# Optimization experiments

Measured on AMD Instinct MI355X. Metric: run time of the kernel, lower is better.

The kernel has to match this reference:

```python
import jax, jax.numpy as jnp
import numpy as np

# Static module configuration (RT-DETR defaults, 640x640 input pyramid)
SPATIAL_SHAPES = ((80, 80), (40, 40), (20, 20))
N_HEADS = 8
N_LEVELS = 3
N_POINTS = 4
D_MODEL = 256
HEAD_DIM = D_MODEL // N_HEADS
OFFSET_SCALE = 0.5
LP = N_LEVELS * N_POINTS


def setup_inputs() -> dict:
    key = jax.random.key(0)
    ks = jax.random.split(key, 10)
    B, Q = 16, 300
    S = sum(h * w for h, w in SPATIAL_SHAPES)  # 8400

    def w(k, shape, scale=0.02):
        return jax.random.normal(k, shape, jnp.float32) * scale

    return {
        "hidden_states": jax.random.normal(ks[0], (B, Q, D_MODEL), jnp.float32),
        "encoder_hidden_states": jax.random.normal(ks[1], (B, S, D_MODEL), jnp.float32),
        # (cx, cy, w, h) boxes in (0,1); 4-coordinate RTDETRv2 path
        "reference_points": jax.random.uniform(ks[2], (B, Q, 1, 4), jnp.float32, 0.1, 0.9),
        "w_value": w(ks[3], (D_MODEL, D_MODEL)),
        "b_value": jnp.zeros((D_MODEL,), jnp.float32),
        "w_offsets": w(ks[4], (N_HEADS * LP * 2, D_MODEL)),
        "b_offsets": w(ks[5], (N_HEADS * LP * 2,), 0.5),
        "w_attn": w(ks[6], (N_HEADS * LP, D_MODEL)),
        "b_attn": jnp.zeros((N_HEADS * LP,), jnp.float32),
        "w_out": w(ks[7], (D_MODEL, D_MODEL)),
        "b_out": jnp.zeros((D_MODEL,), jnp.float32),
    }


def _bilinear_sample(img, gx, gy):
    """grid_sample(mode=bilinear, padding_mode=zeros, align_corners=False).
    img: [N, C, H, W]; gx, gy: [N, Q, P] absolute pixel coords (already W*loc-0.5).
    Returns [N, Q, P, C]."""
    N, C, H, W = img.shape
    x0 = jnp.floor(gx)
    y0 = jnp.floor(gy)
    x1 = x0 + 1.0
    y1 = y0 + 1.0
    wx1 = gx - x0
    wx0 = 1.0 - wx1
    wy1 = gy - y0
    wy0 = 1.0 - wy1
    b = jnp.arange(N)[:, None, None]

    def gather(ix, iy):
        valid = (ix >= 0) & (ix < W) & (iy >= 0) & (iy < H)
        ixc = jnp.clip(ix, 0, W - 1).astype(jnp.int32)
        iyc = jnp.clip(iy, 0, H - 1).astype(jnp.int32)
        v = img[b, :, iyc, ixc]  # [N,Q,P,C]
        return v * valid[..., None].astype(img.dtype)

    return (gather(x0, y0) * (wx0 * wy0)[..., None]
            + gather(x1, y0) * (wx1 * wy0)[..., None]
            + gather(x0, y1) * (wx0 * wy1)[..., None]
            + gather(x1, y1) * (wx1 * wy1)[..., None])


def _msda_v2(hidden_states, encoder_hidden_states, reference_points,
             w_value, b_value, w_offsets, b_offsets, w_attn, b_attn, w_out, b_out):
    B, Q, _ = hidden_states.shape
    S = encoder_hidden_states.shape[1]

    value = (encoder_hidden_states @ w_value.T + b_value).reshape(B, S, N_HEADS, HEAD_DIM)
    offsets = (hidden_states @ w_offsets.T + b_offsets).reshape(B, Q, N_HEADS, LP, 2)
    attn = jax.nn.softmax(
        (hidden_states @ w_attn.T + b_attn).reshape(B, Q, N_HEADS, LP), axis=-1)

    # n_points_scale = [1/P]*L*P; 4-coordinate reference points (cx,cy,w,h)
    n_points_scale = jnp.float32(1.0 / N_POINTS)
    offset = offsets * n_points_scale * reference_points[:, :, None, :, 2:] * OFFSET_SCALE
    loc = reference_points[:, :, None, :, :2] + offset  # [B,Q,H,LP,2] in (0,1)

    # head-major value: [B*H, hd, S]
    v = value.transpose(0, 2, 3, 1).reshape(B * N_HEADS, HEAD_DIM, S)
    grids = loc.transpose(0, 2, 1, 3, 4).reshape(B * N_HEADS, Q, LP, 2)

    sampled = []
    start = 0
    for lvl, (H, W) in enumerate(SPATIAL_SHAPES):
        vl = v[:, :, start:start + H * W].reshape(B * N_HEADS, HEAD_DIM, H, W)
        g = grids[:, :, lvl * N_POINTS:(lvl + 1) * N_POINTS, :]
        # torch: grid = 2*loc-1 with align_corners=False -> pixel = loc*W - 0.5
        gx = g[..., 0] * W - 0.5
        gy = g[..., 1] * H - 0.5
        sampled.append(_bilinear_sample(vl, gx, gy))  # [B*H, Q, P, hd]
        start += H * W

    sv = jnp.concatenate(sampled, axis=2)  # [B*H, Q, LP, hd]
    aw = attn.transpose(0, 2, 1, 3).reshape(B * N_HEADS, Q, LP, 1)
    out = (sv * aw).sum(axis=2)  # [B*H, Q, hd]
    out = out.reshape(B, N_HEADS, Q, HEAD_DIM).transpose(0, 2, 1, 3).reshape(B, Q, D_MODEL)
    return out @ w_out.T + b_out


def reference(hidden_states, encoder_hidden_states, reference_points,
              w_value, b_value, w_offsets, b_offsets, w_attn, b_attn, w_out, b_out):
    return _msda_v2(hidden_states, encoder_hidden_states, reference_points,
                    w_value, b_value, w_offsets, b_offsets, w_attn, b_attn, w_out, b_out)
```

## Files before the change

### kernel.cpp

```cpp
#include <hip/hip_runtime.h>


typedef __attribute__((ext_vector_type(8))) short short8;
typedef __attribute__((ext_vector_type(4))) float f32x4;

__device__ __forceinline__ unsigned short f2bf(float f) {
    union { float f; unsigned int i; } v; v.f = f;
    unsigned int r = v.i + 0x7FFFu + ((v.i >> 16) & 1u);
    return (unsigned short)(r >> 16);
}
__device__ __forceinline__ float bf2f(unsigned short u) {
    union { unsigned int i; float f; } v;
    v.i = ((unsigned int)u) << 16;
    return v.f;
}
__device__ __forceinline__ short8 cvt8(const float* p) {
    f32x4 x = *(const f32x4*)p;
    f32x4 y = *(const f32x4*)(p + 4);
    short8 r;
#pragma unroll
    for (int q = 0; q < 4; ++q) {
        r[q]     = (short)f2bf(x[q]);
        r[q + 4] = (short)f2bf(y[q]);
    }
    return r;
}
__device__ __forceinline__ void barrier_lgkm() {
    asm volatile("s_waitcnt lgkmcnt(0)\n\ts_barrier" ::: "memory");
}

__global__ __launch_bounds__(256) void prep_kernel(
    const float* __restrict__ wv, const float* __restrict__ wo,
    const float* __restrict__ w_off, const float* __restrict__ w_attn,
    short8* __restrict__ wv_s, short8* __restrict__ wo_s, short8* __restrict__ wp_s)
{
    const int blk = blockIdx.x, tid = threadIdx.x;
    if (blk < 64) {
        const float* W = (blk < 32) ? wv : wo;
        short8* out    = (blk < 32) ? wv_s : wo_s;
        int s   = ((blk & 31) << 8) + tid;
        int kcb = s >> 10, sl = s & 1023;
        int n = ((sl >> 6) << 4) + (sl & 15);
        int k = (kcb << 5) + (((sl >> 4) & 3) << 3);
        out[s] = cvt8(W + n * 256 + k);
    } else {
        int s   = ((blk - 64) << 8) + tid;
        int kcb = s / 1152, sl = s - kcb * 1152;
        int n = ((sl >> 6) << 4) + (sl & 15);
        int k = (kcb << 5) + (((sl >> 4) & 3) << 3);
        const float* p = (n < 192) ? (w_off + (size_t)n * 256 + k)
                                   : (w_attn + (size_t)(n - 192) * 256 + k);
        wp_s[s] = cvt8(p);
    }
}

__global__ __launch_bounds__(256) void gemm128(
    const float* __restrict__ A,
    const short8* __restrict__ Wswz,
    const float* __restrict__ bias,
    unsigned short* __restrict__ C)
{
    __shared__ short8 lb[1024];
    const int tid  = threadIdx.x;
    const int wave = tid >> 6;
    const int lane = tid & 63;
    const int row0 = (blockIdx.x >> 1) * 128;
    const int colt = blockIdx.x & 1;
    const int mq   = wave >> 1;
    const int nq   = wave & 1;

    f32x4 acc[4][4];
#pragma unroll
    for (int i = 0; i < 4; ++i)
#pragma unroll
        for (int j = 0; j < 4; ++j) acc[i][j] = (f32x4){0.f, 0.f, 0.f, 0.f};

    const int sa0 = tid, sa1 = tid + 256;
    const int am0 = row0 + ((sa0 >> 6) << 4) + (sa0 & 15);
    const int ak0 = ((sa0 >> 4) & 3) << 3;
    const int am1 = row0 + ((sa1 >> 6) << 4) + (sa1 & 15);
    const int ak1 = ((sa1 >> 4) & 3) << 3;

    for (int kcb = 0; kcb < 8; ++kcb) {
        const int kc = kcb << 5;
        barrier_lgkm();
        lb[sa0] = cvt8(A + (size_t)am0 * 256 + kc + ak0);
        lb[sa1] = cvt8(A + (size_t)am1 * 256 + kc + ak1);
        const short8* wsrc = Wswz + (kcb << 10) + (colt << 9);
        lb[512 + tid]       = wsrc[tid];
        lb[768 + tid]       = wsrc[tid + 256];
        barrier_lgkm();

        short8 af[4], bf[4];
#pragma unroll
        for (int i = 0; i < 4; ++i) af[i] = lb[((mq << 2) + i) * 64 + lane];
#pragma unroll
        for (int j = 0; j < 4; ++j) bf[j] = lb[512 + ((nq << 2) + j) * 64 + lane];
#pragma unroll
        for (int i = 0; i < 4; ++i)
#pragma unroll
            for (int j = 0; j < 4; ++j)
                acc[i][j] = __builtin_amdgcn_mfma_f32_16x16x32_bf16(af[i], bf[j], acc[i][j], 0, 0, 0);
    }

    const int ncol = lane & 15;
    const int rsub = (lane >> 4) << 2;
#pragma unroll
    for (int i = 0; i < 4; ++i) {
        const int rb = row0 + ((mq << 2) + i) * 16 + rsub;
#pragma unroll
        for (int j = 0; j < 4; ++j) {
            const int n = (colt << 7) + ((nq << 2) + j) * 16 + ncol;
            const float bv = bias[n];
#pragma unroll
            for (int r = 0; r < 4; ++r)
                C[(size_t)(rb + r) * 256 + n] = f2bf(acc[i][j][r] + bv);
        }
    }
}

template <bool A_BF16, bool OUT_BF16>
__global__ __launch_bounds__(256) void gemm_nt(
    const void* __restrict__ Av,
    const short8* __restrict__ Wswz,
    const float* __restrict__ bias,
    void* __restrict__ Cv)
{
    __shared__ short8 lb[2048];
    const int tid  = threadIdx.x;
    const int wave = tid >> 6;
    const int lane = tid & 63;
    const int row0 = blockIdx.x * 64 + wave * 16;

    f32x4 acc[16];
#pragma unroll
    for (int t = 0; t < 16; ++t) acc[t] = (f32x4){0.f, 0.f, 0.f, 0.f};

    const int am = row0 + (lane & 15);
    const int kq = (lane >> 4) << 3;

    const unsigned short* Ab = (const unsigned short*)Av;
    const float*          Af = (const float*)Av;

    short8 acur[2], anext[2];
#pragma unroll
    for (int kk = 0; kk < 2; ++kk) {
        if (A_BF16) acur[kk] = *(const short8*)(Ab + (size_t)am * 256 + (kk << 5) + kq);
        else        acur[kk] = cvt8(Af + (size_t)am * 256 + (kk << 5) + kq);
    }

    for (int st = 0; st < 4; ++st) {
        barrier_lgkm();
#pragma unroll
        for (int i = 0; i < 8; ++i) {
            int s = tid + (i << 8);
            lb[s] = Wswz[(st << 11) + s];
        }
        barrier_lgkm();

        if (st < 3) {
            int kc = (st + 1) << 6;
#pragma unroll
            for (int kk = 0; kk < 2; ++kk) {
                if (A_BF16) anext[kk] = *(const short8*)(Ab + (size_t)am * 256 + kc + (kk << 5) + kq);
                else        anext[kk] = cvt8(Af + (size_t)am * 256 + kc + (kk << 5) + kq);
            }
        }

#pragma unroll
        for (int t = 0; t < 16; ++t) {
            short8 b0 = lb[t * 64 + lane];
            acc[t] = __builtin_amdgcn_mfma_f32_16x16x32_bf16(acur[0], b0, acc[t], 0, 0, 0);
            short8 b1 = lb[1024 + t * 64 + lane];
            acc[t] = __builtin_amdgcn_mfma_f32_16x16x32_bf16(acur[1], b1, acc[t], 0, 0, 0);
        }
        acur[0] = anext[0];
        acur[1] = anext[1];
    }

    const int ncol = lane & 15;
    const int rb   = row0 + ((lane >> 4) << 2);
#pragma unroll
    for (int t = 0; t < 16; ++t) {
        int n = (t << 4) + ncol;
        float bv = bias[n];
#pragma unroll
        for (int r = 0; r < 4; ++r) {
            float v = acc[t][r] + bv;
            if (OUT_BF16)
                ((unsigned short*)Cv)[(size_t)(rb + r) * 256 + n] = f2bf(v);
            else
                ((float*)Cv)[(size_t)(rb + r) * 256 + n] = v;
        }
    }
}

#define LGS 296
__global__ __launch_bounds__(256) void proj_gemm(
    const float* __restrict__ hidden,
    const short8* __restrict__ Wswz,
    const float* __restrict__ b_off, const float* __restrict__ b_attn,
    const float* __restrict__ refp,
    float* __restrict__ attnw, float* __restrict__ locw)
{
    __shared__ char smem[32 * LGS * 4];
    short8* lb = (short8*)smem;
    float*  lg = (float*)smem;

    const int tid  = threadIdx.x;
    const int wave = tid >> 6;
    const int lane = tid & 63;
    const int rq0  = blockIdx.x * 32;
    const int rg   = wave >> 1;
    const int ts   = (wave & 1) * 9;
    const int row0 = rq0 + rg * 16;

    f32x4 acc[9];
#pragma unroll
    for (int t = 0; t < 9; ++t) acc[t] = (f32x4){0.f, 0.f, 0.f, 0.f};

    const int am = row0 + (lane & 15);
    const int kq = (lane >> 4) << 3;

    for (int kcb = 0; kcb < 8; ++kcb) {
        __syncthreads();
#pragma unroll
        for (int i = 0; i < 5; ++i) {
            int s = tid + (i << 8);
            if (s < 1152) lb[s] = Wswz[kcb * 1152 + s];
        }
        __syncthreads();

        short8 a = cvt8(hidden + (size_t)am * 256 + (kcb << 5) + kq);
#pragma unroll
        for (int t = 0; t < 9; ++t)
            acc[t] = __builtin_amdgcn_mfma_f32_16x16x32_bf16(a, lb[(ts + t) * 64 + lane], acc[t], 0, 0, 0);
    }

    __syncthreads();
    const int ncol = lane & 15;
    const int rb   = rg * 16 + ((lane >> 4) << 2);
#pragma unroll
    for (int t = 0; t < 9; ++t) {
        int n = (ts + t) * 16 + ncol;
        float bv = (n < 192) ? b_off[n] : b_attn[n - 192];
#pragma unroll
        for (int r = 0; r < 4; ++r)
            lg[(rb + r) * LGS + n] = acc[t][r] + bv;
    }
    __syncthreads();

    {
        int r = tid >> 3, h = tid & 7;
        const float* lrow = lg + r * LGS + 192 + h * 12;
        float m = -1e30f;
#pragma unroll
        for (int p = 0; p < 12; ++p) m = fmaxf(m, lrow[p]);
        float e[12], sum = 0.f;
#pragma unroll
        for (int p = 0; p < 12; ++p) { e[p] = __expf(lrow[p] - m); sum += e[p]; }
        float inv = 1.f / sum;
        float* ao = attnw + (size_t)(rq0 + r) * 96 + h * 12;
#pragma unroll
        for (int p = 0; p < 12; ++p) ao[p] = e[p] * inv;
    }
    if (tid < 192) {
        int xy = tid & 1;
        for (int r = 0; r < 32; ++r) {
            int rq = rq0 + r;
            float rc  = refp[(size_t)rq * 4 + xy];
            float rwh = refp[(size_t)rq * 4 + 2 + xy];
            locw[(size_t)rq * 192 + tid] = rc + lg[r * LGS + tid] * 0.125f * rwh;
        }
    }
}

__global__ __launch_bounds__(256) void sample_kernel(
    const unsigned short* __restrict__ value,
    const float* __restrict__ attnw, const float* __restrict__ locw,
    unsigned short* __restrict__ sampled)
{
    const int rq  = blockIdx.x;
    const int b   = rq / 300;
    const int tid = threadIdx.x;

    __shared__ int4   soff[96];
    __shared__ float4 swt[96];

    if (tid < 96) {
        int h = tid / 12, lp = tid - h * 12;
        int l = lp >> 2;
        int Wl = (l == 0) ? 80 : (l == 1) ? 40 : 20;
        int s0 = (l == 0) ? 0  : (l == 1) ? 6400 : 8000;
        float lx = locw[(size_t)rq * 192 + h * 24 + lp * 2];
        float ly = locw[(size_t)rq * 192 + h * 24 + lp * 2 + 1];
        float aw = attnw[(size_t)rq * 96 + h * 12 + lp];
        float gx = lx * (float)Wl - 0.5f;
        float gy = ly * (float)Wl - 0.5f;
        float x0f = floorf(gx), y0f = floorf(gy);
        int   x0 = (int)x0f,   y0 = (int)y0f;
        float wx1 = gx - x0f, wx0 = 1.f - wx1;
        float wy1 = gy - y0f, wy0 = 1.f - wy1;
        int4 of; float4 wt;
#pragma unroll
        for (int j = 0; j < 4; ++j) {
            int x = x0 + (j & 1), y = y0 + (j >> 1);
            bool ok = (x >= 0) & (x < Wl) & (y >= 0) & (y < Wl);
            int idx = ok ? (((b * 8400 + s0 + y * Wl + x) * 8 + h) * 32) : 0;
            float w = ok ? aw * ((j & 1) ? wx1 : wx0) * ((j >> 1) ? wy1 : wy0) : 0.f;
            ((int*)&of)[j] = idx;
            ((float*)&wt)[j] = w;
        }
        soff[tid] = of;
        swt[tid]  = wt;
    }
    __syncthreads();

    const int h = tid >> 5, c = tid & 31;
    float acc = 0.f;
#pragma unroll
    for (int lp = 0; lp < 12; ++lp) {
        int idx = h * 12 + lp;
        int4   of = soff[idx];
        float4 wt = swt[idx];
        acc += wt.x * bf2f(value[of.x + c]);
        acc += wt.y * bf2f(value[of.y + c]);
        acc += wt.z * bf2f(value[of.z + c]);
        acc += wt.w * bf2f(value[of.w + c]);
    }
    sampled[(size_t)rq * 256 + tid] = f2bf(acc);
}

extern "C" void kernel_launch(void* const* d_in, const int* in_sizes, int n_in,
                              void* d_out, int out_size, void* d_ws, size_t ws_size,
                              hipStream_t stream)
{
    const float* hidden  = (const float*)d_in[0];
    const float* enc     = (const float*)d_in[1];
    const float* refp    = (const float*)d_in[2];
    const float* w_value = (const float*)d_in[3];
    const float* b_value = (const float*)d_in[4];
    const float* w_off   = (const float*)d_in[5];
    const float* b_off   = (const float*)d_in[6];
    const float* w_attn  = (const float*)d_in[7];
    const float* b_attn  = (const float*)d_in[8];
    const float* w_out   = (const float*)d_in[9];
    const float* b_out   = (const float*)d_in[10];

    char* ws = (char*)d_ws;
    unsigned short* value   = (unsigned short*)ws;
    unsigned short* sampled = (unsigned short*)(ws + 68812800);
    float*          attnw   = (float*)(ws + 71270400);
    float*          locw    = (float*)(ws + 73113600);
    short8*         wv_swz  = (short8*)(ws + 76800000);
    short8*         wo_swz  = (short8*)(ws + 76931072);
    short8*         wp_swz  = (short8*)(ws + 77062144);

    prep_kernel<<<100, 256, 0, stream>>>(w_value, w_out, w_off, w_attn,
                                         wv_swz, wo_swz, wp_swz);
    gemm128<<<2100, 256, 0, stream>>>(enc, wv_swz, b_value, value);
    proj_gemm<<<150, 256, 0, stream>>>(hidden, wp_swz, b_off, b_attn,
                                       refp, attnw, locw);
    sample_kernel<<<4800, 256, 0, stream>>>(value, attnw, locw, sampled);
    gemm_nt<true, false><<<75, 256, 0, stream>>>(sampled, wo_swz, b_out,
                                                 d_out);
}
```

Measured before the change: 298.6 us.

## Prefetch next A tile into registers and load weights directly into LDS

In the bf16 MFMA projection GEMM, the fp32 A-tile loads for the next k-block are issued into registers before the current block's MFMAs. The pre-swizzled weight tile is moved with global_load_lds DMA instead of going through registers. Hand-written s_waitcnt vmcnt counts let the prefetch stay in flight across the barrier. This is meant to hide global load latency in the K loop, at the cost of fragile manual waitcnt accounting and more registers in use.

```diff
diff --git a/kernel.cpp b/kernel.cpp
--- a/kernel.cpp
+++ b/kernel.cpp
@@ -25,8 +25,22 @@
     }
     return r;
 }
+__device__ __forceinline__ short8 pack8(f32x4 x, f32x4 y) {
+    short8 r;
+#pragma unroll
+    for (int q = 0; q < 4; ++q) {
+        r[q]     = (short)f2bf(x[q]);
+        r[q + 4] = (short)f2bf(y[q]);
+    }
+    return r;
+}
 __device__ __forceinline__ void barrier_lgkm() {
     asm volatile("s_waitcnt lgkmcnt(0)\n\ts_barrier" ::: "memory");
+}
+__device__ __forceinline__ void gload_lds16(const void* g, void* l) {
+    __builtin_amdgcn_global_load_lds(
+        (const __attribute__((address_space(1))) void*)g,
+        (__attribute__((address_space(3))) void*)l, 16, 0, 0);
 }
 
 __global__ __launch_bounds__(256) void prep_kernel(
@@ -81,15 +95,41 @@
     const int am1 = row0 + ((sa1 >> 6) << 4) + (sa1 & 15);
     const int ak1 = ((sa1 >> 4) & 3) << 3;
 
+    const float* pa0 = A + (size_t)am0 * 256 + ak0;
+    const float* pa1 = A + (size_t)am1 * 256 + ak1;
+
+    f32x4 a00 = *(const f32x4*)(pa0);
+    f32x4 a01 = *(const f32x4*)(pa0 + 4);
+    f32x4 a10 = *(const f32x4*)(pa1);
+    f32x4 a11 = *(const f32x4*)(pa1 + 4);
+
+    const int wv64 = wave << 6;
+    const short8* wcol = Wswz + (colt << 9);
+    short8* ldsB0 = &lb[512 + wv64];
+    short8* ldsB1 = &lb[768 + wv64];
+
     for (int kcb = 0; kcb < 8; ++kcb) {
-        const int kc = kcb << 5;
-        barrier_lgkm();
-        lb[sa0] = cvt8(A + (size_t)am0 * 256 + kc + ak0);
-        lb[sa1] = cvt8(A + (size_t)am1 * 256 + kc + ak1);
-        const short8* wsrc = Wswz + (kcb << 10) + (colt << 9);
-        lb[512 + tid]       = wsrc[tid];
-        lb[768 + tid]       = wsrc[tid + 256];
-        barrier_lgkm();
+        __builtin_amdgcn_s_barrier();
+
+        lb[sa0] = pack8(a00, a01);
+        lb[sa1] = pack8(a10, a11);
+
+        const short8* wsrc = wcol + (kcb << 10) + wv64 + lane;
+        gload_lds16(wsrc,       ldsB0);
+        gload_lds16(wsrc + 256, ldsB1);
+        asm volatile("" ::: "memory");
+
+        if (kcb < 7) {
+            const float* q0 = pa0 + ((kcb + 1) << 5);
+            const float* q1 = pa1 + ((kcb + 1) << 5);
+            a00 = *(const f32x4*)(q0);
+            a01 = *(const f32x4*)(q0 + 4);
+            a10 = *(const f32x4*)(q1);
+            a11 = *(const f32x4*)(q1 + 4);
+            asm volatile("s_waitcnt vmcnt(4) lgkmcnt(0)\n\ts_barrier" ::: "memory");
+        } else {
+            asm volatile("s_waitcnt vmcnt(0) lgkmcnt(0)\n\ts_barrier" ::: "memory");
+        }
 
         short8 af[4], bf[4];
 #pragma unroll
```

New measurement: 296.7 us. No clear change (-0.6%).

## Vectorize bilinear gather over 4 queries per block and split output GEMM columns

Applied to the files above, without the earlier changes.

The sampling kernel now processes four queries per block, with each lane loading four bf16 channels at once via 8-byte loads and writing a packed 4-element result. This reduces the number of load instructions and the per-block setup overhead of the gather. The output projection GEMM is split into two column halves per row tile, doubling the block count to improve CU occupancy. The cost is fewer threads per channel group and a duplicated A-tile load across the column halves.

```diff
diff --git a/kernel.cpp b/kernel.cpp
--- a/kernel.cpp
+++ b/kernel.cpp
@@ -2,6 +2,7 @@
 
 
 typedef __attribute__((ext_vector_type(8))) short short8;
+typedef __attribute__((ext_vector_type(4))) short short4v;
 typedef __attribute__((ext_vector_type(4))) float f32x4;
 
 __device__ __forceinline__ unsigned short f2bf(float f) {
@@ -126,15 +127,16 @@
     const float* __restrict__ bias,
     void* __restrict__ Cv)
 {
-    __shared__ short8 lb[2048];
+    __shared__ short8 lb[1024];
     const int tid  = threadIdx.x;
     const int wave = tid >> 6;
     const int lane = tid & 63;
-    const int row0 = blockIdx.x * 64 + wave * 16;
-
-    f32x4 acc[16];
-#pragma unroll
-    for (int t = 0; t < 16; ++t) acc[t] = (f32x4){0.f, 0.f, 0.f, 0.f};
+    const int row0 = (blockIdx.x >> 1) * 64 + wave * 16;
+    const int colt = blockIdx.x & 1;
+
+    f32x4 acc[8];
+#pragma unroll
+    for (int t = 0; t < 8; ++t) acc[t] = (f32x4){0.f, 0.f, 0.f, 0.f};
 
     const int am = row0 + (lane & 15);
     const int kq = (lane >> 4) << 3;
@@ -152,9 +154,10 @@
     for (int st = 0; st < 4; ++st) {
         barrier_lgkm();
 #pragma unroll
-        for (int i = 0; i < 8; ++i) {
-            int s = tid + (i << 8);
-            lb[s] = Wswz[(st << 11) + s];
+        for (int i = 0; i < 4; ++i) {
+            int s  = tid + (i << 8);
+            int kk = s >> 9, r = s & 511;
+            lb[s] = Wswz[(((st << 1) + kk) << 10) + (colt << 9) + r];
         }
         barrier_lgkm();
 
@@ -168,10 +171,10 @@
         }
 
 #pragma unroll
-        for (int t = 0; t < 16; ++t) {
+        for (int t = 0; t < 8; ++t) {
             short8 b0 = lb[t * 64 + lane];
             acc[t] = __builtin_amdgcn_mfma_f32_16x16x32_bf16(acur[0], b0, acc[t], 0, 0, 0);
-            short8 b1 = lb[1024 + t * 64 + lane];
+            short8 b1 = lb[512 + t * 64 + lane];
             acc[t] = __builtin_amdgcn_mfma_f32_16x16x32_bf16(acur[1], b1, acc[t], 0, 0, 0);
         }
         acur[0] = anext[0];
@@ -181,8 +184,8 @@
     const int ncol = lane & 15;
     const int rb   = row0 + ((lane >> 4) << 2);
 #pragma unroll
-    for (int t = 0; t < 16; ++t) {
-        int n = (t << 4) + ncol;
+    for (int t = 0; t < 8; ++t) {
+        int n = (colt << 7) + (t << 4) + ncol;
         float bv = bias[n];
 #pragma unroll
         for (int r = 0; r < 4; ++r) {
@@ -280,16 +283,19 @@
     const float* __restrict__ attnw, const float* __restrict__ locw,
     unsigned short* __restrict__ sampled)
 {
-    const int rq  = blockIdx.x;
-    const int b   = rq / 300;
+    const int rq0 = blockIdx.x << 2;
     const int tid = threadIdx.x;
 
-    __shared__ int4   soff[96];
-    __shared__ float4 swt[96];
-
-    if (tid < 96) {
-        int h = tid / 12, lp = tid - h * 12;
-        int l = lp >> 2;
+    __shared__ int4   soff[4][96];
+    __shared__ float4 swt[4][96];
+
+    for (int it = tid; it < 384; it += 256) {
+        int rsub = it / 96;
+        int idx  = it - rsub * 96;
+        int rq   = rq0 + rsub;
+        int b    = rq / 300;
+        int h  = idx / 12, lp = idx - h * 12;
+        int l  = lp >> 2;
         int Wl = (l == 0) ? 80 : (l == 1) ? 40 : 20;
         int s0 = (l == 0) ? 0  : (l == 1) ? 6400 : 8000;
         float lx = locw[(size_t)rq * 192 + h * 24 + lp * 2];
@@ -306,29 +312,46 @@
         for (int j = 0; j < 4; ++j) {
             int x = x0 + (j & 1), y = y0 + (j >> 1);
             bool ok = (x >= 0) & (x < Wl) & (y >= 0) & (y < Wl);
-            int idx = ok ? (((b * 8400 + s0 + y * Wl + x) * 8 + h) * 32) : 0;
+            int idx2 = ok ? (((b * 8400 + s0 + y * Wl + x) * 8 + h) * 32) : 0;
             float w = ok ? aw * ((j & 1) ? wx1 : wx0) * ((j >> 1) ? wy1 : wy0) : 0.f;
-            ((int*)&of)[j] = idx;
+            ((int*)&of)[j] = idx2;
             ((float*)&wt)[j] = w;
         }
-        soff[tid] = of;
-        swt[tid]  = wt;
+        soff[rsub][idx] = of;
+        swt[rsub][idx]  = wt;
     }
     __syncthreads();
 
-    const int h = tid >> 5, c = tid & 31;
-    float acc = 0.f;
+    const int rsub = tid >> 6;
+    const int lane = tid & 63;
+    const int h    = lane >> 3;
+    const int cq   = (lane & 7) << 2;
+    const int rq   = rq0 + rsub;
+
+    float acc0 = 0.f, acc1 = 0.f, acc2 = 0.f, acc3 = 0.f;
+    const int base = h * 12;
 #pragma unroll
     for (int lp = 0; lp < 12; ++lp) {
-        int idx = h * 12 + lp;
-        int4   of = soff[idx];
-        float4 wt = swt[idx];
-        acc += wt.x * bf2f(value[of.x + c]);
-        acc += wt.y * bf2f(value[of.y + c]);
-        acc += wt.z * bf2f(value[of.z + c]);
-        acc += wt.w * bf2f(value[of.w + c]);
-    }
-    sampled[(size_t)rq * 256 + tid] = f2bf(acc);
+        int4   of = soff[rsub][base + lp];
+        float4 wt = swt[rsub][base + lp];
+#pragma unroll
+        for (int j = 0; j < 4; ++j) {
+            int   o = ((const int*)&of)[j];
+            float w = ((const float*)&wt)[j];
+            uint2 u = *(const uint2*)(value + o + cq);
+            union { unsigned int i; float f; } c0, c1, c2, c3;
+            c0.i = u.x << 16; c1.i = u.x & 0xFFFF0000u;
+            c2.i = u.y << 16; c3.i = u.y & 0xFFFF0000u;
+            acc0 += w * c0.f; acc1 += w * c1.f;
+            acc2 += w * c2.f; acc3 += w * c3.f;
+        }
+    }
+    short4v out;
+    out[0] = (short)f2bf(acc0);
+    out[1] = (short)f2bf(acc1);
+    out[2] = (short)f2bf(acc2);
+    out[3] = (short)f2bf(acc3);
+    *(short4v*)(sampled + (size_t)rq * 256 + h * 32 + cq) = out;
 }
 
 extern "C" void kernel_launch(void* const* d_in, const int* in_sizes, int n_in,
@@ -361,7 +384,7 @@
     gemm128<<<2100, 256, 0, stream>>>(enc, wv_swz, b_value, value);
     proj_gemm<<<150, 256, 0, stream>>>(hidden, wp_swz, b_off, b_attn,
                                        refp, attnw, locw);
-    sample_kernel<<<4800, 256, 0, stream>>>(value, attnw, locw, sampled);
-    gemm_nt<true, false><<<75, 256, 0, stream>>>(sampled, wo_swz, b_out,
-                                                 d_out);
-}
+    sample_kernel<<<1200, 256, 0, stream>>>(value, attnw, locw, sampled);
+    gemm_nt<true, false><<<150, 256, 0, stream>>>(sampled, wo_swz, b_out,
+                                                  d_out);
+}
```

After: 289.8 us. 2.9% less time.
